# Kernel tuning notes

Measured on AMD Instinct MI355X. Metric: run time of the kernel, lower is better.

Reference implementation:

```python
import jax, jax.numpy as jnp
import numpy as np

N, IN_DIM, OUT_DIM = 262144, 512, 128


def setup_inputs() -> dict:
    key = jax.random.key(0)
    k1, k2, k3, k4 = jax.random.split(key, 4)
    x = jax.random.normal(k1, (N, IN_DIM), dtype=jnp.float32)
    mask = jax.random.normal(k2, (N,), dtype=jnp.float32)
    # nn.Linear params: W [out_dim, in_dim], b [out_dim]
    bound = 1.0 / np.sqrt(IN_DIM)
    W = jax.random.uniform(k3, (OUT_DIM, IN_DIM), dtype=jnp.float32, minval=-bound, maxval=bound)
    b = jax.random.uniform(k4, (OUT_DIM,), dtype=jnp.float32, minval=-bound, maxval=bound)
    return {"x": x, "mask": mask, "W": W, "b": b}


def reference(x, mask, W, b):
    # Linear: out = x @ W^T + b  -> [N, out_dim]
    out = jnp.einsum("ni,oi->no", x, W) + b
    # threshold = mean over rows of per-row sums (scalar)
    threshold = out.sum(axis=1).mean()
    # stream compaction: indices where mask > threshold.
    # jit-compatible fixed-size output padded with -1 (original returns a
    # data-dependent [K, 1] int tensor via np.argwhere).
    idx = jnp.argwhere(mask > threshold, size=mask.shape[0], fill_value=-1)
    return out, idx
```

## Files before the change

### kernel.cpp

```cpp
#include <hip/hip_runtime.h>

#define NROWS 262144
#define KDIM  512
#define ODIM  128

typedef __attribute__((ext_vector_type(8))) __bf16 bf16x8;
typedef __attribute__((ext_vector_type(4))) float  f32x4;

typedef __attribute__((address_space(1))) const unsigned int* gas_u32p;
typedef __attribute__((address_space(3))) unsigned int*       las_u32p;


__global__ __launch_bounds__(256) void convert_w_kernel(
    const float* __restrict__ W, char* __restrict__ WpB) {
  int gid = blockIdx.x * 256 + threadIdx.x;
  int kg = gid & 3, r = (gid >> 2) & 127, kc = gid >> 9;
  const float4* src = (const float4*)(W + (size_t)r * KDIM + kc * 32 + kg * 8);
  float4 v0 = src[0], v1 = src[1];
  float f[8] = {v0.x, v0.y, v0.z, v0.w, v1.x, v1.y, v1.z, v1.w};
  bf16x8 h, l;
#pragma unroll
  for (int e = 0; e < 8; ++e) {
    __bf16 hh = (__bf16)f[e];
    h[e] = hh;
    l[e] = (__bf16)(f[e] - (float)hh);
  }
  char* slice = WpB + (size_t)kc * 16384 + r * 128;
  int swz = r & 7;
  *(bf16x8*)(slice + ((kg ^ swz)) * 16)       = h;
  *(bf16x8*)(slice + (((4 + kg) ^ swz)) * 16) = l;
}

__global__ __launch_bounds__(256, 3) void gemm_kernel(
    const float* __restrict__ x, const char* __restrict__ WpB,
    const float* __restrict__ bias, float* __restrict__ out,
    double* __restrict__ partials) {
  const int lane = threadIdx.x & 63;
  const int wid  = threadIdx.x >> 6;
  const int ncol = lane & 15;
  const int kg   = lane >> 4;

  __shared__ __align__(16) char lds[49152];

  const int row0 = blockIdx.x * 128 + wid * 32 + ncol;
  const float* xrow0 = x + (size_t)row0 * KDIM + kg * 8;
  const float* xrow1 = xrow0 + (size_t)16 * KDIM;

  f32x4 acc[2][8];
#pragma unroll
  for (int rs = 0; rs < 2; ++rs)
#pragma unroll
    for (int ct = 0; ct < 8; ++ct) acc[rs][ct] = (f32x4){0.f, 0.f, 0.f, 0.f};

  float a_cur[2][8];
#pragma unroll
  for (int rs = 0; rs < 2; ++rs) {
    const float4* p = (const float4*)(rs ? xrow1 : xrow0);
    float4 v0 = p[0], v1 = p[1];
    a_cur[rs][0] = v0.x; a_cur[rs][1] = v0.y; a_cur[rs][2] = v0.z; a_cur[rs][3] = v0.w;
    a_cur[rs][4] = v1.x; a_cur[rs][5] = v1.y; a_cur[rs][6] = v1.z; a_cur[rs][7] = v1.w;
  }
#pragma unroll
  for (int s = 0; s < 2; ++s) {
#pragma unroll
    for (int i = 0; i < 4; ++i) {
      const int cbase = (wid * 4 + i) * 64;
      __builtin_amdgcn_global_load_lds(
          (gas_u32p)(WpB + (size_t)s * 16384 + (size_t)(cbase + lane) * 16),
          (las_u32p)(lds + s * 16384 + cbase * 16), 16, 0, 0);
    }
  }

  int cb = 0;
  int sb = 2;
#pragma unroll 2
  for (int kc = 0; kc < 16; ++kc) {
    float a_nxt[2][8];
    {
      const int kn = (kc < 15) ? (kc * 32 + 32) : kc * 32;
#pragma unroll
      for (int rs = 0; rs < 2; ++rs) {
        const float4* p = (const float4*)((rs ? xrow1 : xrow0) + kn);
        float4 v0 = p[0], v1 = p[1];
        a_nxt[rs][0] = v0.x; a_nxt[rs][1] = v0.y; a_nxt[rs][2] = v0.z; a_nxt[rs][3] = v0.w;
        a_nxt[rs][4] = v1.x; a_nxt[rs][5] = v1.y; a_nxt[rs][6] = v1.z; a_nxt[rs][7] = v1.w;
      }
    }
    asm volatile("s_waitcnt vmcnt(8)" ::: "memory");
    asm volatile("s_barrier" ::: "memory");

    bf16x8 ah[2], al[2];
#pragma unroll
    for (int rs = 0; rs < 2; ++rs)
#pragma unroll
      for (int e = 0; e < 8; ++e) {
        float f = a_cur[rs][e];
        __bf16 h = (__bf16)f;
        ah[rs][e] = h;
        al[rs][e] = (__bf16)(f - (float)h);
      }
    const char* cur = lds + cb * 16384;
#pragma unroll
    for (int ct = 0; ct < 8; ++ct) {
      const int r   = ct * 16 + ncol;
      const int swz = r & 7;
      bf16x8 bh = *(const bf16x8*)(cur + (size_t)(r * 8 + (kg ^ swz)) * 16);
      bf16x8 bl = *(const bf16x8*)(cur + (size_t)(r * 8 + ((4 + kg) ^ swz)) * 16);
#pragma unroll
      for (int rs = 0; rs < 2; ++rs) {
        acc[rs][ct] = __builtin_amdgcn_mfma_f32_16x16x32_bf16(ah[rs], bh, acc[rs][ct], 0, 0, 0);
        acc[rs][ct] = __builtin_amdgcn_mfma_f32_16x16x32_bf16(al[rs], bh, acc[rs][ct], 0, 0, 0);
        acc[rs][ct] = __builtin_amdgcn_mfma_f32_16x16x32_bf16(ah[rs], bl, acc[rs][ct], 0, 0, 0);
      }
    }
    {
      const char* gsrc = WpB + (size_t)((kc + 2) & 15) * 16384;
      char* dst = lds + sb * 16384;
#pragma unroll
      for (int i = 0; i < 4; ++i) {
        const int cbase = (wid * 4 + i) * 64;
        __builtin_amdgcn_global_load_lds(
            (gas_u32p)(gsrc + (size_t)(cbase + lane) * 16),
            (las_u32p)(dst + cbase * 16), 16, 0, 0);
      }
    }
#pragma unroll
    for (int rs = 0; rs < 2; ++rs)
#pragma unroll
      for (int e = 0; e < 8; ++e) a_cur[rs][e] = a_nxt[rs][e];
    cb = (cb == 2) ? 0 : cb + 1;
    sb = (sb == 2) ? 0 : sb + 1;
  }

  double lsum = 0.0;
#pragma unroll
  for (int rs = 0; rs < 2; ++rs) {
    const int orow0 = blockIdx.x * 128 + wid * 32 + rs * 16 + kg * 4;
#pragma unroll
    for (int ct = 0; ct < 8; ++ct) {
      float bv = bias[ct * 16 + ncol];
#pragma unroll
      for (int r = 0; r < 4; ++r) {
        float v = acc[rs][ct][r] + bv;
        out[(size_t)(orow0 + r) * ODIM + ct * 16 + ncol] = v;
        lsum += (double)v;
      }
    }
  }
#pragma unroll
  for (int off = 32; off; off >>= 1) lsum += __shfl_xor(lsum, off);
  __shared__ double wpart[4];
  if (lane == 0) wpart[wid] = lsum;
  __syncthreads();
  if (threadIdx.x == 0)
    partials[blockIdx.x] = wpart[0] + wpart[1] + wpart[2] + wpart[3];
}

__device__ inline float compute_threshold(const double* __restrict__ partials,
                                          double* __restrict__ red) {
  double s = 0.0;
  for (int j = threadIdx.x; j < 2048; j += 256) s += partials[j];
  red[threadIdx.x] = s;
  __syncthreads();
  for (int st = 128; st; st >>= 1) {
    if ((int)threadIdx.x < st) red[threadIdx.x] += red[threadIdx.x + st];
    __syncthreads();
  }
  return (float)(red[0] / (double)NROWS);
}

__global__ __launch_bounds__(256) void count_kernel(
    const float* __restrict__ mask, const double* __restrict__ partials,
    int* __restrict__ counts, float* __restrict__ idx_out) {
  __shared__ double red[256];
  float thr = compute_threshold(partials, red);

  int base = blockIdx.x * 1024 + threadIdx.x * 4;
  float4 m = *(const float4*)(mask + base);
  int c = (m.x > thr) + (m.y > thr) + (m.z > thr) + (m.w > thr);
  *(float4*)(idx_out + base) = (float4){-1.f, -1.f, -1.f, -1.f};

  __shared__ int ired[256];
  ired[threadIdx.x] = c;
  __syncthreads();
  for (int st = 128; st; st >>= 1) {
    if ((int)threadIdx.x < st) ired[threadIdx.x] += ired[threadIdx.x + st];
    __syncthreads();
  }
  if (threadIdx.x == 0) counts[blockIdx.x] = ired[0];
}

__global__ __launch_bounds__(256) void scan_kernel(
    const int* __restrict__ counts, int* __restrict__ offsets) {
  __shared__ int tmp[256];
  int tid = threadIdx.x;
  int v = counts[tid];
  tmp[tid] = v;
  __syncthreads();
#pragma unroll
  for (int st = 1; st < 256; st <<= 1) {
    int t = (tid >= st) ? tmp[tid - st] : 0;
    __syncthreads();
    tmp[tid] += t;
    __syncthreads();
  }
  offsets[tid] = tmp[tid] - v;
}

__global__ __launch_bounds__(256) void scatter_kernel(
    const float* __restrict__ mask, const double* __restrict__ partials,
    const int* __restrict__ offsets, float* __restrict__ idx_out) {
  __shared__ double red[256];
  float thr = compute_threshold(partials, red);

  int base = blockIdx.x * 1024 + threadIdx.x * 4;
  float4 m = *(const float4*)(mask + base);
  int p0 = m.x > thr, p1 = m.y > thr, p2 = m.z > thr, p3 = m.w > thr;
  int tc = p0 + p1 + p2 + p3;

  int lane = threadIdx.x & 63, wv = threadIdx.x >> 6;
  int incl = tc;
#pragma unroll
  for (int off = 1; off < 64; off <<= 1) {
    int v = __shfl_up(incl, off);
    if (lane >= off) incl += v;
  }
  __shared__ int wsum[4];
  if (lane == 63) wsum[wv] = incl;
  __syncthreads();
  int wbase = 0;
  for (int w = 0; w < wv; ++w) wbase += wsum[w];

  int pos = offsets[blockIdx.x] + wbase + (incl - tc);
  if (p0) idx_out[pos++] = (float)(base + 0);
  if (p1) idx_out[pos++] = (float)(base + 1);
  if (p2) idx_out[pos++] = (float)(base + 2);
  if (p3) idx_out[pos++] = (float)(base + 3);
}

extern "C" void kernel_launch(void* const* d_in, const int* in_sizes, int n_in,
                              void* d_out, int out_size, void* d_ws, size_t ws_size,
                              hipStream_t stream) {
  const float* x    = (const float*)d_in[0];
  const float* mask = (const float*)d_in[1];
  const float* W    = (const float*)d_in[2];
  const float* bias = (const float*)d_in[3];

  float* out     = (float*)d_out;
  float* idx_out = out + (size_t)NROWS * ODIM;

  char*   ws       = (char*)d_ws;
  char*   WpB      = ws;
  double* partials = (double*)(ws + 262144);
  int*    counts   = (int*)(ws + 278528);
  int*    offsets  = (int*)(ws + 279552);

  convert_w_kernel<<<32, 256, 0, stream>>>(W, WpB);
  gemm_kernel<<<2048, 256, 0, stream>>>(x, WpB, bias, out, partials);
  count_kernel<<<256, 256, 0, stream>>>(mask, partials, counts, idx_out);
  scan_kernel<<<1, 256, 0, stream>>>(counts, offsets);
  scatter_kernel<<<256, 256, 0, stream>>>(mask, partials, offsets, idx_out);
}
```

Measured before the change: 755.2 us.

## Prefetch two K-chunks of x per iteration with restructured wait counts

The GEMM main loop is restructured to process two 32-wide K chunks per iteration. It issues x loads for both upcoming chunks together, so each float4 pair covers 64 contiguous K values across the lane groups, and it adjusts the vmcnt waits to match. The aim is wider, more coalesced global reads of x and fewer load/wait round trips. In exchange, register pressure rises from doubled a_cur/a_nxt buffers, and the hand-tuned vmcnt counts must line up with the interleaved W LDS loads.

```diff
diff --git a/kernel.cpp b/kernel.cpp
--- a/kernel.cpp
+++ b/kernel.cpp
@@ -52,13 +52,17 @@
 #pragma unroll
     for (int ct = 0; ct < 8; ++ct) acc[rs][ct] = (f32x4){0.f, 0.f, 0.f, 0.f};
 
-  float a_cur[2][8];
+  float a_cur[2][16], a_nxt[2][16];
+
 #pragma unroll
   for (int rs = 0; rs < 2; ++rs) {
     const float4* p = (const float4*)(rs ? xrow1 : xrow0);
-    float4 v0 = p[0], v1 = p[1];
-    a_cur[rs][0] = v0.x; a_cur[rs][1] = v0.y; a_cur[rs][2] = v0.z; a_cur[rs][3] = v0.w;
-    a_cur[rs][4] = v1.x; a_cur[rs][5] = v1.y; a_cur[rs][6] = v1.z; a_cur[rs][7] = v1.w;
+    float4 q0 = p[0], q1 = p[1];
+    float4 q2 = p[8], q3 = p[9];
+    a_cur[rs][0]=q0.x; a_cur[rs][1]=q0.y; a_cur[rs][2]=q0.z; a_cur[rs][3]=q0.w;
+    a_cur[rs][4]=q1.x; a_cur[rs][5]=q1.y; a_cur[rs][6]=q1.z; a_cur[rs][7]=q1.w;
+    a_cur[rs][8]=q2.x; a_cur[rs][9]=q2.y; a_cur[rs][10]=q2.z; a_cur[rs][11]=q2.w;
+    a_cur[rs][12]=q3.x; a_cur[rs][13]=q3.y; a_cur[rs][14]=q3.z; a_cur[rs][15]=q3.w;
   }
 #pragma unroll
   for (int s = 0; s < 2; ++s) {
@@ -74,47 +78,49 @@
   int cb = 0;
   int sb = 2;
 #pragma unroll 2
-  for (int kc = 0; kc < 16; ++kc) {
-    float a_nxt[2][8];
-    {
-      const int kn = (kc < 15) ? (kc * 32 + 32) : kc * 32;
+  for (int s = 0; s < 8; ++s) {
+    asm volatile("s_waitcnt vmcnt(4)" ::: "memory");
+    asm volatile("s_barrier" ::: "memory");
+    {
+      bf16x8 ah[2], al[2];
+#pragma unroll
+      for (int rs = 0; rs < 2; ++rs)
+#pragma unroll
+        for (int e = 0; e < 8; ++e) {
+          float f = a_cur[rs][e];
+          __bf16 h = (__bf16)f;
+          ah[rs][e] = h;
+          al[rs][e] = (__bf16)(f - (float)h);
+        }
+      const char* cur = lds + cb * 16384;
+#pragma unroll
+      for (int ct = 0; ct < 8; ++ct) {
+        const int r   = ct * 16 + ncol;
+        const int swz = r & 7;
+        bf16x8 bh = *(const bf16x8*)(cur + (size_t)(r * 8 + (kg ^ swz)) * 16);
+        bf16x8 bl = *(const bf16x8*)(cur + (size_t)(r * 8 + ((4 + kg) ^ swz)) * 16);
+#pragma unroll
+        for (int rs = 0; rs < 2; ++rs) {
+          acc[rs][ct] = __builtin_amdgcn_mfma_f32_16x16x32_bf16(ah[rs], bh, acc[rs][ct], 0, 0, 0);
+          acc[rs][ct] = __builtin_amdgcn_mfma_f32_16x16x32_bf16(al[rs], bh, acc[rs][ct], 0, 0, 0);
+          acc[rs][ct] = __builtin_amdgcn_mfma_f32_16x16x32_bf16(ah[rs], bl, acc[rs][ct], 0, 0, 0);
+        }
+      }
+    }
+    {
+      const int coff = ((s < 7) ? (s + 1) : 7) * 64;
 #pragma unroll
       for (int rs = 0; rs < 2; ++rs) {
-        const float4* p = (const float4*)((rs ? xrow1 : xrow0) + kn);
-        float4 v0 = p[0], v1 = p[1];
-        a_nxt[rs][0] = v0.x; a_nxt[rs][1] = v0.y; a_nxt[rs][2] = v0.z; a_nxt[rs][3] = v0.w;
-        a_nxt[rs][4] = v1.x; a_nxt[rs][5] = v1.y; a_nxt[rs][6] = v1.z; a_nxt[rs][7] = v1.w;
-      }
-    }
-    asm volatile("s_waitcnt vmcnt(8)" ::: "memory");
-    asm volatile("s_barrier" ::: "memory");
-
-    bf16x8 ah[2], al[2];
-#pragma unroll
-    for (int rs = 0; rs < 2; ++rs)
-#pragma unroll
-      for (int e = 0; e < 8; ++e) {
-        float f = a_cur[rs][e];
-        __bf16 h = (__bf16)f;
-        ah[rs][e] = h;
-        al[rs][e] = (__bf16)(f - (float)h);
-      }
-    const char* cur = lds + cb * 16384;
-#pragma unroll
-    for (int ct = 0; ct < 8; ++ct) {
-      const int r   = ct * 16 + ncol;
-      const int swz = r & 7;
-      bf16x8 bh = *(const bf16x8*)(cur + (size_t)(r * 8 + (kg ^ swz)) * 16);
-      bf16x8 bl = *(const bf16x8*)(cur + (size_t)(r * 8 + ((4 + kg) ^ swz)) * 16);
-#pragma unroll
-      for (int rs = 0; rs < 2; ++rs) {
-        acc[rs][ct] = __builtin_amdgcn_mfma_f32_16x16x32_bf16(ah[rs], bh, acc[rs][ct], 0, 0, 0);
-        acc[rs][ct] = __builtin_amdgcn_mfma_f32_16x16x32_bf16(al[rs], bh, acc[rs][ct], 0, 0, 0);
-        acc[rs][ct] = __builtin_amdgcn_mfma_f32_16x16x32_bf16(ah[rs], bl, acc[rs][ct], 0, 0, 0);
-      }
-    }
-    {
-      const char* gsrc = WpB + (size_t)((kc + 2) & 15) * 16384;
+        const float4* p = (const float4*)((rs ? xrow1 : xrow0) + coff);
+        float4 q0 = p[0], q1 = p[1], q2 = p[8], q3 = p[9];
+        a_nxt[rs][0]=q0.x; a_nxt[rs][1]=q0.y; a_nxt[rs][2]=q0.z; a_nxt[rs][3]=q0.w;
+        a_nxt[rs][4]=q1.x; a_nxt[rs][5]=q1.y; a_nxt[rs][6]=q1.z; a_nxt[rs][7]=q1.w;
+        a_nxt[rs][8]=q2.x; a_nxt[rs][9]=q2.y; a_nxt[rs][10]=q2.z; a_nxt[rs][11]=q2.w;
+        a_nxt[rs][12]=q3.x; a_nxt[rs][13]=q3.y; a_nxt[rs][14]=q3.z; a_nxt[rs][15]=q3.w;
+      }
+    }
+    {
+      const char* gsrc = WpB + (size_t)((2 * s + 2) & 15) * 16384;
       char* dst = lds + sb * 16384;
 #pragma unroll
       for (int i = 0; i < 4; ++i) {
@@ -124,10 +130,52 @@
             (las_u32p)(dst + cbase * 16), 16, 0, 0);
       }
     }
+    cb = (cb == 2) ? 0 : cb + 1;
+    sb = (sb == 2) ? 0 : sb + 1;
+
+    asm volatile("s_waitcnt vmcnt(12)" ::: "memory");
+    asm volatile("s_barrier" ::: "memory");
+    {
+      bf16x8 ah[2], al[2];
+#pragma unroll
+      for (int rs = 0; rs < 2; ++rs)
+#pragma unroll
+        for (int e = 0; e < 8; ++e) {
+          float f = a_cur[rs][8 + e];
+          __bf16 h = (__bf16)f;
+          ah[rs][e] = h;
+          al[rs][e] = (__bf16)(f - (float)h);
+        }
+      const char* cur = lds + cb * 16384;
+#pragma unroll
+      for (int ct = 0; ct < 8; ++ct) {
+        const int r   = ct * 16 + ncol;
+        const int swz = r & 7;
+        bf16x8 bh = *(const bf16x8*)(cur + (size_t)(r * 8 + (kg ^ swz)) * 16);
+        bf16x8 bl = *(const bf16x8*)(cur + (size_t)(r * 8 + ((4 + kg) ^ swz)) * 16);
+#pragma unroll
+        for (int rs = 0; rs < 2; ++rs) {
+          acc[rs][ct] = __builtin_amdgcn_mfma_f32_16x16x32_bf16(ah[rs], bh, acc[rs][ct], 0, 0, 0);
+          acc[rs][ct] = __builtin_amdgcn_mfma_f32_16x16x32_bf16(al[rs], bh, acc[rs][ct], 0, 0, 0);
+          acc[rs][ct] = __builtin_amdgcn_mfma_f32_16x16x32_bf16(ah[rs], bl, acc[rs][ct], 0, 0, 0);
+        }
+      }
+    }
+    {
+      const char* gsrc = WpB + (size_t)((2 * s + 3) & 15) * 16384;
+      char* dst = lds + sb * 16384;
+#pragma unroll
+      for (int i = 0; i < 4; ++i) {
+        const int cbase = (wid * 4 + i) * 64;
+        __builtin_amdgcn_global_load_lds(
+            (gas_u32p)(gsrc + (size_t)(cbase + lane) * 16),
+            (las_u32p)(dst + cbase * 16), 16, 0, 0);
+      }
+    }
 #pragma unroll
     for (int rs = 0; rs < 2; ++rs)
 #pragma unroll
-      for (int e = 0; e < 8; ++e) a_cur[rs][e] = a_nxt[rs][e];
+      for (int e = 0; e < 16; ++e) a_cur[rs][e] = a_nxt[rs][e];
     cb = (cb == 2) ? 0 : cb + 1;
     sb = (sb == 2) ? 0 : sb + 1;
   }
```

New measurement: 872.9 us. 15.6% more time.
